# Kernel tuning notes

Measured on AMD Instinct MI355X. Metric: run time of the kernel, lower is better.

## Reference

```python
import jax, jax.numpy as jnp
import numpy as np

N, E = 20000, 160000
H, C1, C_OUT, D_IN = 4, 256, 512, 128
HID = H * C1  # 1024


def gat_conv(x, src, dst, W, a_src, a_dst, b, heads, ch, concat):
    n = x.shape[0]
    xw = (x @ W).reshape(n, heads, ch)                     # [N,H,C]
    es = jnp.sum(xw * a_src, axis=-1)                      # [N,H]
    ed = jnp.sum(xw * a_dst, axis=-1)                      # [N,H]
    e = jax.nn.leaky_relu(es[src] + ed[dst], 0.2)          # [Etot,H]
    m = jax.ops.segment_max(e, dst, num_segments=n)
    m = jnp.where(jnp.isfinite(m), m, 0.0)
    p = jnp.exp(e - m[dst])
    denom = jax.ops.segment_sum(p, dst, num_segments=n)
    alpha = p / (denom[dst] + 1e-16)                       # segment softmax
    out = jax.ops.segment_sum(alpha[:, :, None] * xw[src], dst, num_segments=n)
    out = out.reshape(n, heads * ch) if concat else out.mean(axis=1)
    return out + b


def layer_norm(x, g, b, eps=1e-5):
    mu = jnp.mean(x, axis=-1, keepdims=True)
    var = jnp.var(x, axis=-1, keepdims=True)
    return (x - mu) * jax.lax.rsqrt(var + eps) * g + b


def setup_inputs() -> dict:
    key = jax.random.key(0)
    ks = jax.random.split(key, 16)
    s1, s2, s3 = (2.0 / D_IN) ** 0.5, (2.0 / HID) ** 0.5, (2.0 / HID) ** 0.5
    return {
        "x": jax.random.normal(ks[0], (N, D_IN), jnp.float32),
        "edge_index": jax.random.randint(ks[1], (2, E), 0, N, jnp.int64),
        "W1": jax.random.normal(ks[2], (D_IN, H * C1), jnp.float32) * s1,
        "a_src1": jax.random.normal(ks[3], (H, C1), jnp.float32) * 0.1,
        "a_dst1": jax.random.normal(ks[4], (H, C1), jnp.float32) * 0.1,
        "b1": jnp.zeros((HID,), jnp.float32),
        "ln1_g": jnp.ones((HID,), jnp.float32),
        "ln1_b": jnp.zeros((HID,), jnp.float32),
        "W2": jax.random.normal(ks[5], (HID, H * C1), jnp.float32) * s2,
        "a_src2": jax.random.normal(ks[6], (H, C1), jnp.float32) * 0.1,
        "a_dst2": jax.random.normal(ks[7], (H, C1), jnp.float32) * 0.1,
        "b2": jnp.zeros((HID,), jnp.float32),
        "ln2_g": jnp.ones((HID,), jnp.float32),
        "ln2_b": jnp.zeros((HID,), jnp.float32),
        "W3": jax.random.normal(ks[8], (HID, C_OUT), jnp.float32) * s3,
        "a_src3": jax.random.normal(ks[9], (1, C_OUT), jnp.float32) * 0.1,
        "a_dst3": jax.random.normal(ks[10], (1, C_OUT), jnp.float32) * 0.1,
        "b3": jnp.zeros((C_OUT,), jnp.float32),
    }


def reference(x, edge_index, W1, a_src1, a_dst1, b1, ln1_g, ln1_b,
              W2, a_src2, a_dst2, b2, ln2_g, ln2_b,
              W3, a_src3, a_dst3, b3):
    # add self loops (PyG GATConv default add_self_loops=True)
    loops = jnp.arange(N, dtype=edge_index.dtype)
    src = jnp.concatenate([edge_index[0], loops])
    dst = jnp.concatenate([edge_index[1], loops])

    h = gat_conv(x, src, dst, W1, a_src1, a_dst1, b1, H, C1, True)
    h = jax.nn.elu(layer_norm(h, ln1_g, ln1_b))  # dropout: eval mode (identity)
    h = gat_conv(h, src, dst, W2, a_src2, a_dst2, b2, H, C1, True)
    h = jax.nn.elu(layer_norm(h, ln2_g, ln2_b))
    out = gat_conv(h, src, dst, W3, a_src3, a_dst3, b3, 1, C_OUT, True)
    return out
```

## Files before the change

### kernel.cpp

```cpp
#include <hip/hip_runtime.h>
#include <hip/hip_bf16.h>

typedef __hip_bfloat16 bf16;
typedef __attribute__((ext_vector_type(8))) short short8;
typedef __attribute__((ext_vector_type(4))) float float4v;

#define NN 20000
#define EE 160000
#define ET (NN + EE)

__device__ __forceinline__ float bf2f(bf16 v){ return __bfloat162float(v); }
__device__ __forceinline__ float raw2f(unsigned short u){ return __uint_as_float(((unsigned)u) << 16); }
__device__ __forceinline__ unsigned short f2raw(float f){
  bf16 h = __float2bfloat16(f);
  return *(unsigned short*)&h;
}

struct Ptrs { const void* p[18]; int n[18]; };

__global__ void k_detect(Ptrs P, int* __restrict__ flags){
  int b = blockIdx.x;
  int t = threadIdx.x;
  if (b == 1){
    const int* e = (const int*)P.p[1];
    int odd = e[2*t + 1];
    unsigned long long m2 = __ballot(odd != 0);
    if (t == 0){ flags[1] = (m2 == 0ULL) ? 1 : 0; }
    return;
  }
  const unsigned* w = (const unsigned*)P.p[b];
  int nwords = P.n[b] / 2;
  unsigned v = w[t % nwords];
  int e8 = (v >> 7) & 0xFF;
  int looks = (e8 >= 100 && e8 <= 140) ? 1 : 0;
  unsigned long long mz = __ballot(v == 0u);
  unsigned long long ml = __ballot(looks);
  if (t == 0){
    int nz = __popcll(mz);
    int nonz = 64 - nz;
    int nl = __popcll(ml);
    flags[8+b] = (nonz > 0 && 2*nl >= nonz) ? 0 : 1;
  }
}

struct P13 { const void* src[13]; int off[13]; int n[13]; int fi[13]; };
struct PrepArgs {
  const void* xraw; bf16* Xc;
  const void* w1raw; bf16* Wt1;
  const void* w2raw; bf16* Wt2;
  const void* w3raw; bf16* Wt3;
  const int* eiraw; int* eic;
  P13 p13; float* prm;
  int* counts;
  float* esA; float* edA;
  const int* flags;
};

__device__ __forceinline__ void do_transpose(float (*tile)[33], const void* raw,
    bf16* wt, int K, int M, int f, int bx, int by, int t){
  int kb = by*32, mb = bx*32;
  int tx = t & 31, ty = t >> 5;
  for (int r = 0; r < 4; r++){
    int k = kb + ty + r*8;
    int m = mb + tx;
    float v = f ? ((const float*)raw)[(size_t)k*M+m] : bf2f(((const bf16*)raw)[(size_t)k*M+m]);
    tile[ty + r*8][tx] = v;
  }
  __syncthreads();
  for (int r = 0; r < 4; r++){
    int m = mb + ty + r*8;
    int k = kb + tx;
    wt[(size_t)m*K + k] = __float2bfloat16(tile[tx][ty + r*8]);
  }
}

__global__ __launch_bounds__(256) void k_prep(PrepArgs A){
  __shared__ float tile[32][33];
  int b = blockIdx.x, t = threadIdx.x;
  const int* flags = A.flags;
  if (b < 10000){
    int i = b*256 + t;
    if (flags[8+0]) A.Xc[i] = __float2bfloat16(((const float*)A.xraw)[i]);
    else            A.Xc[i] = ((const bf16*)A.xraw)[i];
  } else if (b < 10128){
    int r = b - 10000;
    do_transpose(tile, A.w1raw, A.Wt1, 128, 1024, flags[8+2], r & 31, r >> 5, t);
  } else if (b < 11152){
    int r = b - 10128;
    do_transpose(tile, A.w2raw, A.Wt2, 1024, 1024, flags[8+8], r & 31, r >> 5, t);
  } else if (b < 11664){
    int r = b - 11152;
    do_transpose(tile, A.w3raw, A.Wt3, 1024, 512, flags[8+14], r & 15, r >> 4, t);
  } else if (b < 12914){
    int i = (b - 11664)*256 + t;
    if (i < 2*EE) A.eic[i] = flags[1] ? A.eiraw[2*i] : A.eiraw[i];
  } else if (b < 12927){
    int pb = b - 12914;
    const void* s = A.p13.src[pb];
    int n = A.p13.n[pb];
    float* d = A.prm + A.p13.off[pb];
    int f = flags[8 + A.p13.fi[pb]];
    for (int i = t; i < n; i += 256)
      d[i] = f ? ((const float*)s)[i] : bf2f(((const bf16*)s)[i]);
  } else if (b < 13006){
    int i = (b - 12927)*256 + t;
    if (i < NN) A.counts[i] = 1;
  } else {
    int i = (b - 13006)*256 + t;
    if (i < NN*4){ A.esA[i] = 0.f; A.edA[i] = 0.f; }
  }
}

__global__ void k_hist(const int* __restrict__ ei, int* __restrict__ counts){
  int e = blockIdx.x*256 + threadIdx.x;
  if (e < EE){
    int d = ei[EE + e];
    if (d >= 0 && d < NN) atomicAdd(&counts[d], 1);
  }
}

__global__ __launch_bounds__(1024) void k_scan(const int* __restrict__ counts, int* __restrict__ rp){
  __shared__ int wsum[16];
  __shared__ int sc;
  int t = threadIdx.x, lane = t & 63, wv = t >> 6;
  if (t == 0) sc = 0;
  __syncthreads();
  for (int base = 0; base < NN; base += 1024){
    int i = base + t;
    int v = (i < NN) ? counts[i] : 0;
    int x = v;
    #pragma unroll
    for (int o = 1; o < 64; o <<= 1){
      int y = __shfl_up(x, o, 64);
      if (lane >= o) x += y;
    }
    if (lane == 63) wsum[wv] = x;
    __syncthreads();
    if (wv == 0 && lane < 16){
      int w = wsum[lane];
      #pragma unroll
      for (int o = 1; o < 16; o <<= 1){
        int y = __shfl_up(w, o, 16);
        if ((lane & 15) >= o) w += y;
      }
      wsum[lane] = w;
    }
    __syncthreads();
    int carry = sc;
    int wpre = (wv > 0) ? wsum[wv-1] : 0;
    if (i < NN) rp[i] = carry + wpre + x - v;
    __syncthreads();
    if (t == 1023) sc = carry + wsum[15];
    __syncthreads();
  }
  if (t == 0) rp[NN] = sc;
}

__global__ void k_selfloop(const int* __restrict__ rp, int* __restrict__ cursor, int* __restrict__ col){
  int i = blockIdx.x*256 + threadIdx.x;
  if (i < NN){ int p = rp[i]; col[p] = i; cursor[i] = p + 1; }
}

__global__ void k_scatter(const int* __restrict__ ei, int* __restrict__ cursor, int* __restrict__ col){
  int e = blockIdx.x*256 + threadIdx.x;
  if (e < EE){
    int s = ei[e], d = ei[EE + e];
    if (d >= 0 && d < NN){
      int pos = atomicAdd(&cursor[d], 1);
      col[pos] = s;
    }
  }
}

__global__ __launch_bounds__(256) void k_gemm_mfma(
    const bf16* __restrict__ X, const bf16* __restrict__ Wt, bf16* __restrict__ Y,
    const float* __restrict__ as_, const float* __restrict__ ad_,
    float* __restrict__ es, float* __restrict__ ed,
    int K, int M, int C, int H)
{
  __shared__ bf16 Xs[128*64];
  __shared__ bf16 Bs[128*64];
  int ncols = gridDim.x;
  int bid = blockIdx.y * ncols + blockIdx.x;
  int xcd  = bid & 7;
  int rest = bid >> 3;
  int colb = rest % ncols;
  int rowb = xcd + 8 * (rest / ncols);
  int r0 = rowb * 128;
  if (r0 >= NN) return;
  int c0 = colb * 128;

  int tid  = threadIdx.x;
  int wave = tid >> 6, lane = tid & 63;
  int quad = lane >> 4, l15 = lane & 15;
  int wr = (wave >> 1) * 64;
  int wc = (wave & 1) * 64;
  int sw = l15 & 7;

  float4v acc[4][4];
  #pragma unroll
  for (int i=0;i<4;i++)
    #pragma unroll
    for (int j=0;j<4;j++)
      acc[i][j] = (float4v){0.f,0.f,0.f,0.f};

  for (int k0 = 0; k0 < K; k0 += 64){
    #pragma unroll
    for (int i = 0; i < 4; i++){
      int ch = i*256 + tid;
      int row = ch >> 3, kl = ch & 7;
      int kg = kl ^ (row & 7);
      const bf16* gx = X  + (size_t)(r0 + row)*K + k0 + kg*8;
      const bf16* gb = Wt + (size_t)(c0 + row)*K + k0 + kg*8;
      __builtin_amdgcn_global_load_lds(
        (const __attribute__((address_space(1))) unsigned int*)gx,
        (__attribute__((address_space(3))) unsigned int*)(Xs + ch*8), 16, 0, 0);
      __builtin_amdgcn_global_load_lds(
        (const __attribute__((address_space(1))) unsigned int*)gb,
        (__attribute__((address_space(3))) unsigned int*)(Bs + ch*8), 16, 0, 0);
    }
    __syncthreads();

    #pragma unroll
    for (int kk = 0; kk < 2; kk++){
      int kp = quad + kk*4;
      short8 af[4], bfr[4];
      #pragma unroll
      for (int i = 0; i < 4; i++){
        int r = wr + i*16 + l15;
        af[i] = *(const short8*)(Xs + ((size_t)r*8 + (kp ^ sw))*8);
      }
      #pragma unroll
      for (int j = 0; j < 4; j++){
        int r = wc + j*16 + l15;
        bfr[j] = *(const short8*)(Bs + ((size_t)r*8 + (kp ^ sw))*8);
      }
      #pragma unroll
      for (int i = 0; i < 4; i++)
        #pragma unroll
        for (int j = 0; j < 4; j++)
          acc[i][j] = __builtin_amdgcn_mfma_f32_16x16x32_bf16(af[i], bfr[j], acc[i][j], 0, 0, 0);
    }
    __syncthreads();
  }

  int h = c0 / C;
  float asv[4], adv[4];
  #pragma unroll
  for (int j = 0; j < 4; j++){
    int colj = c0 + wc + j*16 + l15;
    asv[j] = as_[colj]; adv[j] = ad_[colj];
  }
  #pragma unroll
  for (int i = 0; i < 4; i++){
    int rbase = r0 + wr + i*16 + quad*4;
    #pragma unroll
    for (int rg = 0; rg < 4; rg++){
      int row = rbase + rg;
      bool ok = (row < NN);
      float pe = 0.f, pd = 0.f;
      #pragma unroll
      for (int j = 0; j < 4; j++){
        float v = acc[i][j][rg];
        int colj = c0 + wc + j*16 + l15;
        if (ok) Y[(size_t)row*M + colj] = __float2bfloat16(v);
        pe += v * asv[j];
        pd += v * adv[j];
      }
      #pragma unroll
      for (int o = 1; o < 16; o <<= 1){
        pe += __shfl_xor(pe, o, 64);
        pd += __shfl_xor(pd, o, 64);
      }
      if (ok && l15 == 0){
        atomicAdd(&es[row*H + h], pe);
        atomicAdd(&ed[row*H + h], pd);
      }
    }
  }
}

__global__ __launch_bounds__(256) void k_aggln(const int* __restrict__ rp, const int* __restrict__ col,
    const bf16* __restrict__ xw, const float* __restrict__ es, const float* __restrict__ ed,
    const float* __restrict__ bias, const float* __restrict__ gam, const float* __restrict__ bet,
    bf16* __restrict__ act, float* __restrict__ esz, float* __restrict__ edz, int zn){
  int wv = threadIdx.x >> 6, lane = threadIdx.x & 63;
  int n = blockIdx.x*4 + wv;
  int h = lane >> 4;
  int cb = lane * 16;
  int e0 = rp[n], e1 = rp[n+1], deg = e1 - e0;
  float4 ed4 = *(const float4*)&ed[n*4];
  const unsigned short* xwu = (const unsigned short*)xw;

  float acc[16];
  #pragma unroll
  for (int c=0;c<16;c++) acc[c]=0.f;

  if (deg <= 64){
    int src = 0;
    float l0=-1e30f, l1=-1e30f, l2=-1e30f, l3=-1e30f;
    if (lane < deg){
      src = col[e0 + lane];
      float4 e4 = *(const float4*)&es[src*4];
      float v;
      v = e4.x + ed4.x; l0 = v > 0.f ? v : 0.2f*v;
      v = e4.y + ed4.y; l1 = v > 0.f ? v : 0.2f*v;
      v = e4.z + ed4.z; l2 = v > 0.f ? v : 0.2f*v;
      v = e4.w + ed4.w; l3 = v > 0.f ? v : 0.2f*v;
    }
    float m0=l0, m1=l1, m2=l2, m3=l3;
    #pragma unroll
    for (int o=1;o<64;o<<=1){
      m0 = fmaxf(m0, __shfl_xor(m0,o,64));
      m1 = fmaxf(m1, __shfl_xor(m1,o,64));
      m2 = fmaxf(m2, __shfl_xor(m2,o,64));
      m3 = fmaxf(m3, __shfl_xor(m3,o,64));
    }
    float p0 = (lane<deg) ? __expf(l0-m0) : 0.f;
    float p1 = (lane<deg) ? __expf(l1-m1) : 0.f;
    float p2 = (lane<deg) ? __expf(l2-m2) : 0.f;
    float p3 = (lane<deg) ? __expf(l3-m3) : 0.f;
    float d0=p0, d1=p1, d2=p2, d3=p3;
    #pragma unroll
    for (int o=1;o<64;o<<=1){
      d0 += __shfl_xor(d0,o,64);
      d1 += __shfl_xor(d1,o,64);
      d2 += __shfl_xor(d2,o,64);
      d3 += __shfl_xor(d3,o,64);
    }
    float al0 = p0 * (1.f/(d0+1e-16f));
    float al1 = p1 * (1.f/(d1+1e-16f));
    float al2 = p2 * (1.f/(d2+1e-16f));
    float al3 = p3 * (1.f/(d3+1e-16f));

    for (int j=0;j<deg;j++){
      int s = __shfl(src, j, 64);
      float a0j = __shfl(al0, j, 64);
      float a1j = __shfl(al1, j, 64);
      float a2j = __shfl(al2, j, 64);
      float a3j = __shfl(al3, j, 64);
      float aj = (h==0) ? a0j : ((h==1) ? a1j : ((h==2) ? a2j : a3j));
      const unsigned short* row = xwu + (size_t)s*1024 + cb;
      ushort4 u0 = *(const ushort4*)(row);
      ushort4 u1 = *(const ushort4*)(row+4);
      ushort4 u2 = *(const ushort4*)(row+8);
      ushort4 u3 = *(const ushort4*)(row+12);
      acc[0] += aj*raw2f(u0.x); acc[1] += aj*raw2f(u0.y); acc[2] += aj*raw2f(u0.z); acc[3] += aj*raw2f(u0.w);
      acc[4] += aj*raw2f(u1.x); acc[5] += aj*raw2f(u1.y); acc[6] += aj*raw2f(u1.z); acc[7] += aj*raw2f(u1.w);
      acc[8] += aj*raw2f(u2.x); acc[9] += aj*raw2f(u2.y); acc[10]+= aj*raw2f(u2.z); acc[11]+= aj*raw2f(u2.w);
      acc[12]+= aj*raw2f(u3.x); acc[13]+= aj*raw2f(u3.y); acc[14]+= aj*raw2f(u3.z); acc[15]+= aj*raw2f(u3.w);
    }
  } else {
    float edh = (h==0) ? ed4.x : ((h==1) ? ed4.y : ((h==2) ? ed4.z : ed4.w));
    float m = -1e30f;
    for (int e=e0;e<e1;e++){
      float v = es[col[e]*4 + h] + edh;
      v = v > 0.f ? v : 0.2f*v;
      m = fmaxf(m, v);
    }
    float den = 0.f;
    for (int e=e0;e<e1;e++){
      float v = es[col[e]*4 + h] + edh;
      v = v > 0.f ? v : 0.2f*v;
      den += __expf(v - m);
    }
    float rd = 1.f/(den + 1e-16f);
    for (int e=e0;e<e1;e++){
      int s = col[e];
      float v = es[s*4 + h] + edh;
      v = v > 0.f ? v : 0.2f*v;
      float aj = __expf(v - m) * rd;
      const unsigned short* row = xwu + (size_t)s*1024 + cb;
      ushort4 u0 = *(const ushort4*)(row);
      ushort4 u1 = *(const ushort4*)(row+4);
      ushort4 u2 = *(const ushort4*)(row+8);
      ushort4 u3 = *(const ushort4*)(row+12);
      acc[0] += aj*raw2f(u0.x); acc[1] += aj*raw2f(u0.y); acc[2] += aj*raw2f(u0.z); acc[3] += aj*raw2f(u0.w);
      acc[4] += aj*raw2f(u1.x); acc[5] += aj*raw2f(u1.y); acc[6] += aj*raw2f(u1.z); acc[7] += aj*raw2f(u1.w);
      acc[8] += aj*raw2f(u2.x); acc[9] += aj*raw2f(u2.y); acc[10]+= aj*raw2f(u2.z); acc[11]+= aj*raw2f(u2.w);
      acc[12]+= aj*raw2f(u3.x); acc[13]+= aj*raw2f(u3.y); acc[14]+= aj*raw2f(u3.z); acc[15]+= aj*raw2f(u3.w);
    }
  }

  #pragma unroll
  for (int c=0;c<16;c++) acc[c] += bias[cb+c];
  float s1 = 0.f, s2 = 0.f;
  #pragma unroll
  for (int c=0;c<16;c++){ s1 += acc[c]; s2 += acc[c]*acc[c]; }
  #pragma unroll
  for (int o=1;o<64;o<<=1){
    s1 += __shfl_xor(s1,o,64);
    s2 += __shfl_xor(s2,o,64);
  }
  float mu  = s1 * (1.f/1024.f);
  float var = s2 * (1.f/1024.f) - mu*mu;
  float rstd = rsqrtf(fmaxf(var, 0.f) + 1e-5f);

  ushort4 o4[4];
  #pragma unroll
  for (int q=0;q<4;q++){
    float v0 = (acc[q*4+0]-mu)*rstd*gam[cb+q*4+0] + bet[cb+q*4+0];
    float v1 = (acc[q*4+1]-mu)*rstd*gam[cb+q*4+1] + bet[cb+q*4+1];
    float v2 = (acc[q*4+2]-mu)*rstd*gam[cb+q*4+2] + bet[cb+q*4+2];
    float v3 = (acc[q*4+3]-mu)*rstd*gam[cb+q*4+3] + bet[cb+q*4+3];
    v0 = v0 > 0.f ? v0 : (__expf(v0)-1.f);
    v1 = v1 > 0.f ? v1 : (__expf(v1)-1.f);
    v2 = v2 > 0.f ? v2 : (__expf(v2)-1.f);
    v3 = v3 > 0.f ? v3 : (__expf(v3)-1.f);
    o4[q].x = f2raw(v0); o4[q].y = f2raw(v1); o4[q].z = f2raw(v2); o4[q].w = f2raw(v3);
  }
  unsigned short* dst = (unsigned short*)act + (size_t)n*1024 + cb;
  *(ushort4*)(dst)    = o4[0];
  *(ushort4*)(dst+4)  = o4[1];
  *(ushort4*)(dst+8)  = o4[2];
  *(ushort4*)(dst+12) = o4[3];

  if (lane < zn){ esz[n*zn + lane] = 0.f; edz[n*zn + lane] = 0.f; }
}

__global__ __launch_bounds__(256) void k_agg3(const int* __restrict__ rp, const int* __restrict__ col,
    const bf16* __restrict__ xw, const float* __restrict__ es, const float* __restrict__ ed,
    const float* __restrict__ bias, float* __restrict__ out){
  int wv = threadIdx.x >> 6, lane = threadIdx.x & 63;
  int n = blockIdx.x*4 + wv;
  int cb = lane * 8;
  int e0 = rp[n], e1 = rp[n+1], deg = e1 - e0;
  float edv = ed[n];
  const unsigned short* xwu = (const unsigned short*)xw;

  float acc[8];
  #pragma unroll
  for (int c=0;c<8;c++) acc[c]=0.f;

  if (deg <= 64){
    int src = 0;
    float l = -1e30f;
    if (lane < deg){
      src = col[e0 + lane];
      float v = es[src] + edv;
      l = v > 0.f ? v : 0.2f*v;
    }
    float m = l;
    #pragma unroll
    for (int o=1;o<64;o<<=1) m = fmaxf(m, __shfl_xor(m,o,64));
    float p = (lane<deg) ? __expf(l-m) : 0.f;
    float d = p;
    #pragma unroll
    for (int o=1;o<64;o<<=1) d += __shfl_xor(d,o,64);
    float al = p * (1.f/(d+1e-16f));

    for (int j=0;j<deg;j++){
      int s = __shfl(src, j, 64);
      float aj = __shfl(al, j, 64);
      const unsigned short* row = xwu + (size_t)s*512 + cb;
      ushort4 u0 = *(const ushort4*)(row);
      ushort4 u1 = *(const ushort4*)(row+4);
      acc[0] += aj*raw2f(u0.x); acc[1] += aj*raw2f(u0.y); acc[2] += aj*raw2f(u0.z); acc[3] += aj*raw2f(u0.w);
      acc[4] += aj*raw2f(u1.x); acc[5] += aj*raw2f(u1.y); acc[6] += aj*raw2f(u1.z); acc[7] += aj*raw2f(u1.w);
    }
  } else {
    float m = -1e30f;
    for (int e=e0;e<e1;e++){
      float v = es[col[e]] + edv;
      v = v > 0.f ? v : 0.2f*v;
      m = fmaxf(m, v);
    }
    float den = 0.f;
    for (int e=e0;e<e1;e++){
      float v = es[col[e]] + edv;
      v = v > 0.f ? v : 0.2f*v;
      den += __expf(v - m);
    }
    float rd = 1.f/(den + 1e-16f);
    for (int e=e0;e<e1;e++){
      int s = col[e];
      float v = es[s] + edv;
      v = v > 0.f ? v : 0.2f*v;
      float aj = __expf(v - m) * rd;
      const unsigned short* row = xwu + (size_t)s*512 + cb;
      ushort4 u0 = *(const ushort4*)(row);
      ushort4 u1 = *(const ushort4*)(row+4);
      acc[0] += aj*raw2f(u0.x); acc[1] += aj*raw2f(u0.y); acc[2] += aj*raw2f(u0.z); acc[3] += aj*raw2f(u0.w);
      acc[4] += aj*raw2f(u1.x); acc[5] += aj*raw2f(u1.y); acc[6] += aj*raw2f(u1.z); acc[7] += aj*raw2f(u1.w);
    }
  }
  float* dst = out + (size_t)n*512 + cb;
  #pragma unroll
  for (int c=0;c<8;c++) dst[c] = acc[c] + bias[cb+c];
}

__global__ void k_wssmall(float* __restrict__ out, float code){
  if (threadIdx.x == 0) out[0] = code;
}

extern "C" void kernel_launch(void* const* d_in, const int* in_sizes, int n_in,
                              void* d_out, int out_size, void* d_ws, size_t ws_size,
                              hipStream_t stream){
  float* out = (float*)d_out;
  char* ws = (char*)d_ws;

  static const int EXP_SZ[18] = {2560000, 320000, 131072, 1024,1024,1024,1024,1024,
                                 1048576, 1024,1024,1024,1024,1024,
                                 524288, 512,512,512};
  if (n_in != 18){ k_wssmall<<<1,64,0,stream>>>(out, 500.0f*301.0f); return; }
  for (int i = 0; i < 18; i++)
    if (in_sizes[i] != EXP_SZ[i]){ k_wssmall<<<1,64,0,stream>>>(out, 500.0f*302.0f); return; }
  if (out_size != NN*512){ k_wssmall<<<1,64,0,stream>>>(out, 500.0f*303.0f); return; }
  const size_t NEED = 93215360;
  if (ws_size < NEED){ k_wssmall<<<1,64,0,stream>>>(out, 500.0f*304.0f); return; }

  bf16* xw    = (bf16*) (ws);
  int*  cur   = (int*)  (ws);
  bf16* act   = (bf16*) (ws + 40960000);
  bf16* Xc    = (bf16*) (ws + 81920000);
  float* esC  = (float*)(ws + 81920000);
  float* edC  = (float*)(ws + 82000000);
  bf16* Wt1   = (bf16*) (ws + 87040000);
  bf16* Wt2   = (bf16*) (ws + 87302144);
  bf16* Wt3   = (bf16*) (ws + 89399296);
  float* prm  = (float*)(ws + 90447872);
  int*  flags = (int*)  (ws + 90494976);
  int*  eic   = (int*)  (ws + 90495232);
  float* esB  = (float*)(ws + 90495232);
  float* edB  = (float*)(ws + 90815232);
  float* esA  = (float*)(ws + 91775232);
  float* edA  = (float*)(ws + 92095232);
  int*  rp    = (int*)  (ws + 92415232);
  int*  col   = (int*)  (ws + 92495360);

  float *as1=prm+0, *ad1=prm+1024, *b1=prm+2048, *lg1=prm+3072, *lb1=prm+4096;
  float *as2=prm+5120, *ad2=prm+6144, *b2=prm+7168, *lg2=prm+8192, *lb2=prm+9216;
  float *as3=prm+10240, *ad3=prm+10752, *b3=prm+11264;

  const int TB = 256;
  int gbN = (NN + TB - 1)/TB;
  int gbE = (EE + TB - 1)/TB;

  {
    Ptrs P;
    for (int i=0;i<18;i++){ P.p[i]=d_in[i]; P.n[i]=in_sizes[i]; }
    k_detect<<<18, 64, 0, stream>>>(P, flags);
  }
  {
    PrepArgs A;
    A.xraw = d_in[0]; A.Xc = Xc;
    A.w1raw = d_in[2]; A.Wt1 = Wt1;
    A.w2raw = d_in[8]; A.Wt2 = Wt2;
    A.w3raw = d_in[14]; A.Wt3 = Wt3;
    A.eiraw = (const int*)d_in[1]; A.eic = eic;
    const int idx[13] = {3,4,5,6,7, 9,10,11,12,13, 15,16,17};
    const int off[13] = {0,1024,2048,3072,4096, 5120,6144,7168,8192,9216, 10240,10752,11264};
    const int nn [13] = {1024,1024,1024,1024,1024, 1024,1024,1024,1024,1024, 512,512,512};
    for (int i=0;i<13;i++){ A.p13.src[i]=d_in[idx[i]]; A.p13.off[i]=off[i]; A.p13.n[i]=nn[i]; A.p13.fi[i]=idx[i]; }
    A.prm = prm; A.counts = cur; A.esA = esA; A.edA = edA; A.flags = flags;
    k_prep<<<13006 + 313, TB, 0, stream>>>(A);
  }

  k_hist<<<gbE, TB, 0, stream>>>(eic, cur);
  k_scan<<<1, 1024, 0, stream>>>(cur, rp);
  k_selfloop<<<gbN, TB, 0, stream>>>(rp, cur, col);
  k_scatter<<<gbE, TB, 0, stream>>>(eic, cur, col);

  const int RB = (NN + 127)/128;
  const int R8 = ((RB + 7)/8)*8;
  dim3 g12(1024/128, R8);
  dim3 g3 (512/128,  R8);

  k_gemm_mfma<<<g12, TB, 0, stream>>>(Xc, Wt1, xw, as1, ad1, esA, edA, 128, 1024, 256, 4);
  k_aggln<<<NN/4, TB, 0, stream>>>(rp, col, xw, esA, edA, b1, lg1, lb1, act, esB, edB, 4);

  k_gemm_mfma<<<g12, TB, 0, stream>>>(act, Wt2, xw, as2, ad2, esB, edB, 1024, 1024, 256, 4);
  k_aggln<<<NN/4, TB, 0, stream>>>(rp, col, xw, esB, edB, b2, lg2, lb2, act, esC, edC, 1);

  k_gemm_mfma<<<g3, TB, 0, stream>>>(act, Wt3, xw, as3, ad3, esC, edC, 1024, 512, 512, 1);
  k_agg3<<<NN/4, TB, 0, stream>>>(rp, col, xw, esC, edC, b3, out);
}
```

Baseline: 473.5 us.

## Inline dtype detection into prep, fuse selfloop into scan, unroll aggregation by two

Removes the separate detect kernel by having every prep block compute its own dtype flag with a wave ballot. The self-loop placement is folded into the scan kernel, which now also writes a separate cursor array, so one launch goes away. The gather loops in both aggregation kernels are unrolled by two edges so two row loads are in flight at once. The cost is redundant detection work in every prep block and higher register pressure in the aggregation kernels.

```diff
diff --git a/kernel.cpp b/kernel.cpp
--- a/kernel.cpp
+++ b/kernel.cpp
@@ -16,34 +16,25 @@
   return *(unsigned short*)&h;
 }
 
-struct Ptrs { const void* p[18]; int n[18]; };
-
-__global__ void k_detect(Ptrs P, int* __restrict__ flags){
-  int b = blockIdx.x;
-  int t = threadIdx.x;
-  if (b == 1){
-    const int* e = (const int*)P.p[1];
-    int odd = e[2*t + 1];
-    unsigned long long m2 = __ballot(odd != 0);
-    if (t == 0){ flags[1] = (m2 == 0ULL) ? 1 : 0; }
-    return;
-  }
-  const unsigned* w = (const unsigned*)P.p[b];
-  int nwords = P.n[b] / 2;
-  unsigned v = w[t % nwords];
+__device__ __forceinline__ int detect_f32(const void* raw, int nwords, int lane){
+  unsigned v = ((const unsigned*)raw)[lane % nwords];
   int e8 = (v >> 7) & 0xFF;
   int looks = (e8 >= 100 && e8 <= 140) ? 1 : 0;
   unsigned long long mz = __ballot(v == 0u);
   unsigned long long ml = __ballot(looks);
-  if (t == 0){
-    int nz = __popcll(mz);
-    int nonz = 64 - nz;
-    int nl = __popcll(ml);
-    flags[8+b] = (nonz > 0 && 2*nl >= nonz) ? 0 : 1;
-  }
-}
-
-struct P13 { const void* src[13]; int off[13]; int n[13]; int fi[13]; };
+  int nz = __popcll(mz);
+  int nonz = 64 - nz;
+  int nl = __popcll(ml);
+  return (nonz > 0 && 2*nl >= nonz) ? 0 : 1;
+}
+
+__device__ __forceinline__ int detect_i64(const int* eiraw, int lane){
+  int odd = eiraw[2*lane + 1];
+  unsigned long long m2 = __ballot(odd != 0);
+  return (m2 == 0ULL) ? 1 : 0;
+}
+
+struct P13 { const void* src[13]; int off[13]; int n[13]; };
 struct PrepArgs {
   const void* xraw; bf16* Xc;
   const void* w1raw; bf16* Wt1;
@@ -53,7 +44,6 @@
   P13 p13; float* prm;
   int* counts;
   float* esA; float* edA;
-  const int* flags;
 };
 
 __device__ __forceinline__ void do_transpose(float (*tile)[33], const void* raw,
@@ -77,29 +67,34 @@
 __global__ __launch_bounds__(256) void k_prep(PrepArgs A){
   __shared__ float tile[32][33];
   int b = blockIdx.x, t = threadIdx.x;
-  const int* flags = A.flags;
+  int lane = t & 63;
   if (b < 10000){
+    int f = detect_f32(A.xraw, NN*128/2, lane);
     int i = b*256 + t;
-    if (flags[8+0]) A.Xc[i] = __float2bfloat16(((const float*)A.xraw)[i]);
-    else            A.Xc[i] = ((const bf16*)A.xraw)[i];
+    if (f) A.Xc[i] = __float2bfloat16(((const float*)A.xraw)[i]);
+    else   A.Xc[i] = ((const bf16*)A.xraw)[i];
   } else if (b < 10128){
+    int f = detect_f32(A.w1raw, 128*1024/2, lane);
     int r = b - 10000;
-    do_transpose(tile, A.w1raw, A.Wt1, 128, 1024, flags[8+2], r & 31, r >> 5, t);
+    do_transpose(tile, A.w1raw, A.Wt1, 128, 1024, f, r & 31, r >> 5, t);
   } else if (b < 11152){
+    int f = detect_f32(A.w2raw, 1024*1024/2, lane);
     int r = b - 10128;
-    do_transpose(tile, A.w2raw, A.Wt2, 1024, 1024, flags[8+8], r & 31, r >> 5, t);
+    do_transpose(tile, A.w2raw, A.Wt2, 1024, 1024, f, r & 31, r >> 5, t);
   } else if (b < 11664){
+    int f = detect_f32(A.w3raw, 1024*512/2, lane);
     int r = b - 11152;
-    do_transpose(tile, A.w3raw, A.Wt3, 1024, 512, flags[8+14], r & 15, r >> 4, t);
+    do_transpose(tile, A.w3raw, A.Wt3, 1024, 512, f, r & 15, r >> 4, t);
   } else if (b < 12914){
+    int f64 = detect_i64(A.eiraw, lane);
     int i = (b - 11664)*256 + t;
-    if (i < 2*EE) A.eic[i] = flags[1] ? A.eiraw[2*i] : A.eiraw[i];
+    if (i < 2*EE) A.eic[i] = f64 ? A.eiraw[2*i] : A.eiraw[i];
   } else if (b < 12927){
     int pb = b - 12914;
     const void* s = A.p13.src[pb];
     int n = A.p13.n[pb];
+    int f = detect_f32(s, n/2, lane);
     float* d = A.prm + A.p13.off[pb];
-    int f = flags[8 + A.p13.fi[pb]];
     for (int i = t; i < n; i += 256)
       d[i] = f ? ((const float*)s)[i] : bf2f(((const bf16*)s)[i]);
   } else if (b < 13006){
@@ -119,7 +114,8 @@
   }
 }
 
-__global__ __launch_bounds__(1024) void k_scan(const int* __restrict__ counts, int* __restrict__ rp){
+__global__ __launch_bounds__(1024) void k_scan(const int* __restrict__ counts, int* __restrict__ rp,
+    int* __restrict__ cursor, int* __restrict__ col){
   __shared__ int wsum[16];
   __shared__ int sc;
   int t = threadIdx.x, lane = t & 63, wv = t >> 6;
@@ -148,17 +144,17 @@
     __syncthreads();
     int carry = sc;
     int wpre = (wv > 0) ? wsum[wv-1] : 0;
-    if (i < NN) rp[i] = carry + wpre + x - v;
+    if (i < NN){
+      int p = carry + wpre + x - v;
+      rp[i] = p;
+      col[p] = i;
+      cursor[i] = p + 1;
+    }
     __syncthreads();
     if (t == 1023) sc = carry + wsum[15];
     __syncthreads();
   }
   if (t == 0) rp[NN] = sc;
-}
-
-__global__ void k_selfloop(const int* __restrict__ rp, int* __restrict__ cursor, int* __restrict__ col){
-  int i = blockIdx.x*256 + threadIdx.x;
-  if (i < NN){ int p = rp[i]; col[p] = i; cursor[i] = p + 1; }
 }
 
 __global__ void k_scatter(const int* __restrict__ ei, int* __restrict__ cursor, int* __restrict__ col){
@@ -333,7 +329,36 @@
     float al2 = p2 * (1.f/(d2+1e-16f));
     float al3 = p3 * (1.f/(d3+1e-16f));
 
-    for (int j=0;j<deg;j++){
+    int j = 0;
+    for (; j + 2 <= deg; j += 2){
+      int sA = __shfl(src, j, 64);
+      int sB = __shfl(src, j+1, 64);
+      float a0A = __shfl(al0, j, 64), a1A = __shfl(al1, j, 64);
+      float a2A = __shfl(al2, j, 64), a3A = __shfl(al3, j, 64);
+      float a0B = __shfl(al0, j+1, 64), a1B = __shfl(al1, j+1, 64);
+      float a2B = __shfl(al2, j+1, 64), a3B = __shfl(al3, j+1, 64);
+      float aA = (h==0) ? a0A : ((h==1) ? a1A : ((h==2) ? a2A : a3A));
+      float aB = (h==0) ? a0B : ((h==1) ? a1B : ((h==2) ? a2B : a3B));
+      const unsigned short* rA = xwu + (size_t)sA*1024 + cb;
+      const unsigned short* rB = xwu + (size_t)sB*1024 + cb;
+      ushort4 uA0 = *(const ushort4*)(rA);
+      ushort4 uA1 = *(const ushort4*)(rA+4);
+      ushort4 uA2 = *(const ushort4*)(rA+8);
+      ushort4 uA3 = *(const ushort4*)(rA+12);
+      ushort4 uB0 = *(const ushort4*)(rB);
+      ushort4 uB1 = *(const ushort4*)(rB+4);
+      ushort4 uB2 = *(const ushort4*)(rB+8);
+      ushort4 uB3 = *(const ushort4*)(rB+12);
+      acc[0] += aA*raw2f(uA0.x); acc[1] += aA*raw2f(uA0.y); acc[2] += aA*raw2f(uA0.z); acc[3] += aA*raw2f(uA0.w);
+      acc[4] += aA*raw2f(uA1.x); acc[5] += aA*raw2f(uA1.y); acc[6] += aA*raw2f(uA1.z); acc[7] += aA*raw2f(uA1.w);
+      acc[8] += aA*raw2f(uA2.x); acc[9] += aA*raw2f(uA2.y); acc[10]+= aA*raw2f(uA2.z); acc[11]+= aA*raw2f(uA2.w);
+      acc[12]+= aA*raw2f(uA3.x); acc[13]+= aA*raw2f(uA3.y); acc[14]+= aA*raw2f(uA3.z); acc[15]+= aA*raw2f(uA3.w);
+      acc[0] += aB*raw2f(uB0.x); acc[1] += aB*raw2f(uB0.y); acc[2] += aB*raw2f(uB0.z); acc[3] += aB*raw2f(uB0.w);
+      acc[4] += aB*raw2f(uB1.x); acc[5] += aB*raw2f(uB1.y); acc[6] += aB*raw2f(uB1.z); acc[7] += aB*raw2f(uB1.w);
+      acc[8] += aB*raw2f(uB2.x); acc[9] += aB*raw2f(uB2.y); acc[10]+= aB*raw2f(uB2.z); acc[11]+= aB*raw2f(uB2.w);
+      acc[12]+= aB*raw2f(uB3.x); acc[13]+= aB*raw2f(uB3.y); acc[14]+= aB*raw2f(uB3.z); acc[15]+= aB*raw2f(uB3.w);
+    }
+    for (; j < deg; j++){
       int s = __shfl(src, j, 64);
       float a0j = __shfl(al0, j, 64);
       float a1j = __shfl(al1, j, 64);
@@ -449,7 +474,24 @@
     for (int o=1;o<64;o<<=1) d += __shfl_xor(d,o,64);
     float al = p * (1.f/(d+1e-16f));
 
-    for (int j=0;j<deg;j++){
+    int j = 0;
+    for (; j + 2 <= deg; j += 2){
+      int sA = __shfl(src, j, 64);
+      int sB = __shfl(src, j+1, 64);
+      float aA = __shfl(al, j, 64);
+      float aB = __shfl(al, j+1, 64);
+      const unsigned short* rA = xwu + (size_t)sA*512 + cb;
+      const unsigned short* rB = xwu + (size_t)sB*512 + cb;
+      ushort4 uA0 = *(const ushort4*)(rA);
+      ushort4 uA1 = *(const ushort4*)(rA+4);
+      ushort4 uB0 = *(const ushort4*)(rB);
+      ushort4 uB1 = *(const ushort4*)(rB+4);
+      acc[0] += aA*raw2f(uA0.x); acc[1] += aA*raw2f(uA0.y); acc[2] += aA*raw2f(uA0.z); acc[3] += aA*raw2f(uA0.w);
+      acc[4] += aA*raw2f(uA1.x); acc[5] += aA*raw2f(uA1.y); acc[6] += aA*raw2f(uA1.z); acc[7] += aA*raw2f(uA1.w);
+      acc[0] += aB*raw2f(uB0.x); acc[1] += aB*raw2f(uB0.y); acc[2] += aB*raw2f(uB0.z); acc[3] += aB*raw2f(uB0.w);
+      acc[4] += aB*raw2f(uB1.x); acc[5] += aB*raw2f(uB1.y); acc[6] += aB*raw2f(uB1.z); acc[7] += aB*raw2f(uB1.w);
+    }
+    for (; j < deg; j++){
       int s = __shfl(src, j, 64);
       float aj = __shfl(al, j, 64);
       const unsigned short* row = xwu + (size_t)s*512 + cb;
@@ -510,8 +552,9 @@
   if (ws_size < NEED){ k_wssmall<<<1,64,0,stream>>>(out, 500.0f*304.0f); return; }
 
   bf16* xw    = (bf16*) (ws);
-  int*  cur   = (int*)  (ws);
+  int*  cnt   = (int*)  (ws);
   bf16* act   = (bf16*) (ws + 40960000);
+  int*  cursor= (int*)  (ws + 40960000);
   bf16* Xc    = (bf16*) (ws + 81920000);
   float* esC  = (float*)(ws + 81920000);
   float* edC  = (float*)(ws + 82000000);
@@ -519,7 +562,6 @@
   bf16* Wt2   = (bf16*) (ws + 87302144);
   bf16* Wt3   = (bf16*) (ws + 89399296);
   float* prm  = (float*)(ws + 90447872);
-  int*  flags = (int*)  (ws + 90494976);
   int*  eic   = (int*)  (ws + 90495232);
   float* esB  = (float*)(ws + 90495232);
   float* edB  = (float*)(ws + 90815232);
@@ -533,14 +575,8 @@
   float *as3=prm+10240, *ad3=prm+10752, *b3=prm+11264;
 
   const int TB = 256;
-  int gbN = (NN + TB - 1)/TB;
   int gbE = (EE + TB - 1)/TB;
 
-  {
-    Ptrs P;
-    for (int i=0;i<18;i++){ P.p[i]=d_in[i]; P.n[i]=in_sizes[i]; }
-    k_detect<<<18, 64, 0, stream>>>(P, flags);
-  }
   {
     PrepArgs A;
     A.xraw = d_in[0]; A.Xc = Xc;
@@ -551,15 +587,14 @@
     const int idx[13] = {3,4,5,6,7, 9,10,11,12,13, 15,16,17};
     const int off[13] = {0,1024,2048,3072,4096, 5120,6144,7168,8192,9216, 10240,10752,11264};
     const int nn [13] = {1024,1024,1024,1024,1024, 1024,1024,1024,1024,1024, 512,512,512};
-    for (int i=0;i<13;i++){ A.p13.src[i]=d_in[idx[i]]; A.p13.off[i]=off[i]; A.p13.n[i]=nn[i]; A.p13.fi[i]=idx[i]; }
-    A.prm = prm; A.counts = cur; A.esA = esA; A.edA = edA; A.flags = flags;
+    for (int i=0;i<13;i++){ A.p13.src[i]=d_in[idx[i]]; A.p13.off[i]=off[i]; A.p13.n[i]=nn[i]; }
+    A.prm = prm; A.counts = cnt; A.esA = esA; A.edA = edA;
     k_prep<<<13006 + 313, TB, 0, stream>>>(A);
   }
 
-  k_hist<<<gbE, TB, 0, stream>>>(eic, cur);
-  k_scan<<<1, 1024, 0, stream>>>(cur, rp);
-  k_selfloop<<<gbN, TB, 0, stream>>>(rp, cur, col);
-  k_scatter<<<gbE, TB, 0, stream>>>(eic, cur, col);
+  k_hist<<<gbE, TB, 0, stream>>>(eic, cnt);
+  k_scan<<<1, 1024, 0, stream>>>(cnt, rp, cursor, col);
+  k_scatter<<<gbE, TB, 0, stream>>>(eic, cursor, col);
 
   const int RB = (NN + 127)/128;
   const int R8 = ((RB + 7)/8)*8;
```

Result: no change. 473.5 us (-0.0%).
